# Kernel optimization log

Measured on AMD Instinct MI355X. Metric: run time of the kernel, lower is better.

## Reference

```python
import jax, jax.numpy as jnp
import numpy as np


def _norm(H, add):
    # Faithful port of GTN.norm: transpose, zero diagonal (optionally add self-loop),
    # row-degree inverse scaling, transpose back.
    Ht = H.T
    n = Ht.shape[0]
    eye = jnp.eye(n, dtype=H.dtype)
    Ht = Ht * (1.0 - eye) + (eye if add else 0.0)
    deg = jnp.sum(Ht, axis=1)
    dinv = jnp.where(deg == 0, 0.0, 1.0 / deg)
    return (dinv[:, None] * Ht).T


def _lstm(x, h0, c0, wih, whh, bih, bhh):
    # x: [B, S, D]; single-layer batch_first LSTM, PyTorch gate order (i, f, g, o).
    def step(carry, xt):
        h, c = carry
        gates = xt @ wih.T + h @ whh.T + bih + bhh
        i, f, g, o = jnp.split(gates, 4, axis=-1)
        i = jax.nn.sigmoid(i); f = jax.nn.sigmoid(f)
        g = jnp.tanh(g); o = jax.nn.sigmoid(o)
        c = f * c + i * g
        h = o * jnp.tanh(c)
        return (h, c), h
    (_, _), ys = jax.lax.scan(step, (h0, c0), jnp.transpose(x, (1, 0, 2)))
    return jnp.transpose(ys, (1, 0, 2))  # [B, S, U]


def _forward(A, X, seq_len, seqs, h0, c0, w1a, w1b, w2,
             gcn_w, lin1_w, lin1_b, lstm_wih, lstm_whh, lstm_bih, lstm_bhh, out_w):
    N = A.shape[0]
    B, S, _ = seqs.shape
    A4 = jnp.transpose(A, (2, 0, 1))  # [E, N, N]

    def gtconv(w):  # w: [C, E], softmax over edge-type channels
        return jnp.einsum('enm,ce->cnm', A4, jax.nn.softmax(w, axis=1))

    # layer 0 (first=True): H = conv1(A) @ conv2(A)
    H = jnp.matmul(gtconv(w1a), gtconv(w1b))  # [C, N, N]
    # layer 1: normalize per channel, then H = H_ @ conv1(A)
    Hn = jax.vmap(lambda h: _norm(h, False))(H)
    H = jnp.matmul(Hn, gtconv(w2))

    # gcn_conv per channel: relu(norm(H_c, add=True).T @ (X @ W)), concat over channels
    Hg = jax.vmap(lambda h: _norm(h, True))(H)  # [C, N, N]
    Xw = X @ gcn_w                              # [N, w_out]
    Xc = jax.nn.relu(jnp.einsum('cnm,nw->cmw', Hg, Xw))  # [C, N, w_out]
    X_ = jnp.transpose(Xc, (1, 0, 2)).reshape(N, -1) @ lin1_w.T + lin1_b  # [N, w_out]

    # ragged basket max-pool: masked segment-max over multi-hot baskets
    mask = seqs != 0                                           # [B, S, I]
    pooled = jnp.max(jnp.where(mask[:, :, :, None], X_[None, None], -jnp.inf), axis=2)
    basket_seqs = jnp.where(mask.any(axis=2)[..., None], pooled, 0.0)  # [B, S, w_out]

    lstm_out = _lstm(basket_seqs, h0[0], c0[0], lstm_wih, lstm_whh, lstm_bih, lstm_bhh)
    idx = jnp.clip(seq_len - 1, 0, S - 1)
    actual = lstm_out[jnp.arange(B), idx]      # [B, U]
    return jax.nn.sigmoid(actual @ out_w.T)    # [B, nb_items]


def setup_inputs() -> dict:
    N, E, C, WIN, WOUT, B, S, U = 2048, 4, 2, 64, 64, 16, 20, 256
    I = N  # nb_items
    key = jax.random.key(0)
    ks = jax.random.split(key, 16)
    A = jax.random.uniform(ks[0], (N, N, E), dtype=jnp.float32)
    X = jax.random.normal(ks[1], (N, WIN), dtype=jnp.float32)
    seq_len = jax.random.randint(ks[2], (B,), 1, S + 1)
    # sparse multi-hot baskets (~20 items per basket)
    seqs = (jax.random.uniform(ks[3], (B, S, I)) < 0.01).astype(jnp.int32)
    h0 = jnp.zeros((1, B, U), dtype=jnp.float32)
    c0 = jnp.zeros((1, B, U), dtype=jnp.float32)
    w1a = 0.1 * jax.random.normal(ks[4], (C, E), dtype=jnp.float32)
    w1b = 0.1 * jax.random.normal(ks[5], (C, E), dtype=jnp.float32)
    w2 = 0.1 * jax.random.normal(ks[6], (C, E), dtype=jnp.float32)
    gcn_w = jax.random.normal(ks[7], (WIN, WOUT), dtype=jnp.float32) / np.sqrt(WIN)
    lin1_w = 0.05 * jax.random.normal(ks[8], (WOUT, C * WOUT), dtype=jnp.float32)
    lin1_b = jnp.zeros((WOUT,), dtype=jnp.float32)
    lstm_wih = 0.05 * jax.random.normal(ks[9], (4 * U, WOUT), dtype=jnp.float32)
    lstm_whh = 0.05 * jax.random.normal(ks[10], (4 * U, U), dtype=jnp.float32)
    lstm_bih = jnp.zeros((4 * U,), dtype=jnp.float32)
    lstm_bhh = jnp.zeros((4 * U,), dtype=jnp.float32)
    out_w = 0.05 * jax.random.normal(ks[11], (I, U), dtype=jnp.float32)
    return {"A": A, "X": X, "seq_len": seq_len, "seqs": seqs, "h0": h0, "c0": c0,
            "w1a": w1a, "w1b": w1b, "w2": w2, "gcn_w": gcn_w,
            "lin1_w": lin1_w, "lin1_b": lin1_b, "lstm_wih": lstm_wih,
            "lstm_whh": lstm_whh, "lstm_bih": lstm_bih, "lstm_bhh": lstm_bhh,
            "out_w": out_w}


def reference(A, X, seq_len, seqs, h0, c0, w1a, w1b, w2, gcn_w, lin1_w, lin1_b,
              lstm_wih, lstm_whh, lstm_bih, lstm_bhh, out_w):
    return _forward(A, X, seq_len, seqs, h0, c0, w1a, w1b, w2, gcn_w,
                    lin1_w, lin1_b, lstm_wih, lstm_whh, lstm_bih, lstm_bhh, out_w)
```

## Files before the change

### kernel.cpp

```cpp
#include <hip/hip_runtime.h>
#include <hip/hip_fp16.h>
#include <math.h>

#define NN_ 2048
#define EE_ 4
#define CC_ 2
#define BB_ 16
#define SS_ 20
#define UU_ 256

#define LREGB 80
#define LLDSB 48

typedef __attribute__((ext_vector_type(8))) short short8;
typedef __attribute__((ext_vector_type(4))) float f32x4;
typedef _Float16 half2v __attribute__((ext_vector_type(2)));

__device__ __forceinline__ float sigmoidf_(float x){ return 1.f/(1.f+expf(-x)); }

__device__ __forceinline__ unsigned short f2bf(float x){
    union { float f; unsigned int u; } v; v.f = x;
    unsigned int u = v.u;
    unsigned int r = u + 0x7FFFu + ((u >> 16) & 1u);
    return (unsigned short)(r >> 16);
}

__device__ __forceinline__ half2v u2h2(unsigned int u){
    union { unsigned int u; half2v h; } c; c.u = u; return c.h;
}

__device__ __forceinline__ float dot2f(unsigned int w, unsigned int h, float acc){
#if __has_builtin(__builtin_amdgcn_fdot2)
    return __builtin_amdgcn_fdot2(u2h2(w), u2h2(h), acc, false);
#else
    float w0 = __half2float(__ushort_as_half((unsigned short)(w & 0xffffu)));
    float w1 = __half2float(__ushort_as_half((unsigned short)(w >> 16)));
    float h0f = __half2float(__ushort_as_half((unsigned short)(h & 0xffffu)));
    float h1f = __half2float(__ushort_as_half((unsigned short)(h >> 16)));
    return fmaf(w1, h1f, fmaf(w0, h0f, acc));
#endif
}

__device__ __forceinline__ float sigf(float x){
    x = fminf(fmaxf(x, -30.f), 30.f);
    float e = __builtin_amdgcn_exp2f(-1.442695041f * x);
    return __builtin_amdgcn_rcpf(1.f + e);
}
__device__ __forceinline__ float tanhf_(float x){
    x = fminf(fmaxf(x, -15.f), 15.f);
    float e = __builtin_amdgcn_exp2f(2.885390082f * x);
    return (e - 1.f) * __builtin_amdgcn_rcpf(e + 1.f);
}

typedef const __attribute__((address_space(1))) unsigned int* gas_ptr;
typedef __attribute__((address_space(3))) unsigned int* las_ptr;
__device__ __forceinline__ void gl_lds16(const void* g, void* l){
    __builtin_amdgcn_global_load_lds((gas_ptr)g, (las_ptr)l, 16, 0, 0);
}

__global__ void k_softmax(const float* __restrict__ w1a, const float* __restrict__ w1b,
                          const float* __restrict__ w2, float* __restrict__ sm){
    int t = threadIdx.x;
    if (t < 6){
        int widx = t >> 1, c = t & 1;
        const float* w = (widx==0)? w1a : ((widx==1)? w1b : w2);
        float v[EE_]; float m = -1e30f;
        for (int e=0;e<EE_;e++){ v[e]=w[c*EE_+e]; m=fmaxf(m,v[e]); }
        float s=0.f;
        for (int e=0;e<EE_;e++){ v[e]=expf(v[e]-m); s+=v[e]; }
        for (int e=0;e<EE_;e++) sm[widx*8 + c*4 + e] = v[e]/s;
    }
}

__global__ __launch_bounds__(256) void k_conv_bf16(const float4* __restrict__ A4,
        const float* __restrict__ sm, unsigned short* __restrict__ convA,
        unsigned short* __restrict__ convBT, unsigned short* __restrict__ convCT){
    __shared__ float4 tile[32][33];
    int bx = blockIdx.x*32, by = blockIdx.y*32;
    int tx = threadIdx.x & 31, ty = threadIdx.x >> 5;
    #pragma unroll
    for (int i=0;i<32;i+=8){
        int n = by+ty+i, m = bx+tx;
        float4 a = A4[(size_t)n*NN_ + m];
        tile[ty+i][tx] = a;
        #pragma unroll
        for (int cc=0;cc<CC_;cc++){
            const float* s = sm + cc*4;
            convA[(size_t)cc*NN_*NN_ + (size_t)n*NN_ + m] =
                f2bf(a.x*s[0]+a.y*s[1]+a.z*s[2]+a.w*s[3]);
        }
    }
    __syncthreads();
    #pragma unroll
    for (int i=0;i<32;i+=8){
        int x = bx+ty+i, y = by+tx;
        float4 a = tile[tx][ty+i];
        #pragma unroll
        for (int cc=0;cc<CC_;cc++){
            const float* s1 = sm + 8 + cc*4;
            const float* s2 = sm + 16 + cc*4;
            convBT[(size_t)cc*NN_*NN_ + (size_t)x*NN_ + y] =
                f2bf(a.x*s1[0]+a.y*s1[1]+a.z*s1[2]+a.w*s1[3]);
            convCT[(size_t)cc*NN_*NN_ + (size_t)x*NN_ + y] =
                f2bf(a.x*s2[0]+a.y*s2[1]+a.z*s2[2]+a.w*s2[3]);
        }
    }
}

__global__ __launch_bounds__(256) void k_mfma_gemm(const unsigned short* __restrict__ Abase,
        const unsigned short* __restrict__ Bbase, float* __restrict__ Cbase){
    const int c = blockIdx.z;
    const unsigned short* Ag = Abase + (size_t)c*NN_*NN_;
    const unsigned short* Bg = Bbase + (size_t)c*NN_*NN_;
    float* Cg = Cbase + (size_t)c*NN_*NN_;

    __shared__ __align__(16) unsigned short As[128*32];
    __shared__ __align__(16) unsigned short Bs[128*32];

    const int t = threadIdx.x;
    const int wave = t >> 6, lane = t & 63;
    const int m0 = blockIdx.y*128, n0 = blockIdx.x*128;
    const int wm = wave >> 1, wn = wave & 1;

    f32x4 acc[4][4];
    const f32x4 z = {0.f,0.f,0.f,0.f};
    #pragma unroll
    for (int i=0;i<4;i++)
        #pragma unroll
        for (int j=0;j<4;j++) acc[i][j] = z;

    const int srow = wave*32 + (lane>>2);
    const int scol = (lane&3)*8;
    const unsigned short* agp0 = Ag + (size_t)(m0+srow)*NN_ + scol;
    const unsigned short* agp1 = agp0 + (size_t)16*NN_;
    const unsigned short* bgp0 = Bg + (size_t)(n0+srow)*NN_ + scol;
    const unsigned short* bgp1 = bgp0 + (size_t)16*NN_;
    unsigned short* alp0 = &As[wave*1024];
    unsigned short* alp1 = &As[wave*1024 + 512];
    unsigned short* blp0 = &Bs[wave*1024];
    unsigned short* blp1 = &Bs[wave*1024 + 512];

    const int fr = lane & 15;
    const int fk = (lane >> 4) * 8;

    for (int k0=0; k0<NN_; k0+=32){
        gl_lds16(agp0, alp0);
        gl_lds16(agp1, alp1);
        gl_lds16(bgp0, blp0);
        gl_lds16(bgp1, blp1);
        agp0 += 32; agp1 += 32; bgp0 += 32; bgp1 += 32;
        __syncthreads();
        short8 af[4], bf[4];
        #pragma unroll
        for (int i=0;i<4;i++){
            af[i] = *(const short8*)&As[(wm*64 + i*16 + fr)*32 + fk];
            bf[i] = *(const short8*)&Bs[(wn*64 + i*16 + fr)*32 + fk];
        }
        #pragma unroll
        for (int i=0;i<4;i++)
            #pragma unroll
            for (int j=0;j<4;j++)
                acc[i][j] = __builtin_amdgcn_mfma_f32_16x16x32_bf16(af[i], bf[j], acc[i][j], 0, 0, 0);
        __syncthreads();
    }

    #pragma unroll
    for (int i=0;i<4;i++){
        int row = m0 + wm*64 + i*16 + (lane>>4)*4;
        #pragma unroll
        for (int j=0;j<4;j++){
            int col = n0 + wn*64 + j*16 + (lane & 15);
            #pragma unroll
            for (int r=0;r<4;r++)
                Cg[(size_t)(row+r)*NN_ + col] = acc[i][j][r];
        }
    }
}

__global__ __launch_bounds__(256) void k_hn(const float* __restrict__ H1,
        const float* __restrict__ dinv, unsigned short* __restrict__ Hn){
    int id = blockIdx.x*256 + threadIdx.x;
    int c = id >> 20;
    int rem = id & ((NN_*NN_/4)-1);
    int m = rem >> 9;
    int k4 = (rem & (NN_/4 - 1)) * 4;
    float4 h = *(const float4*)&H1[(size_t)c*NN_*NN_ + (size_t)m*NN_ + k4];
    float4 d = *(const float4*)&dinv[c*NN_ + k4];
    ushort4 o;
    o.x = f2bf((m==k4  ) ? 0.f : h.x*d.x);
    o.y = f2bf((m==k4+1) ? 0.f : h.y*d.y);
    o.z = f2bf((m==k4+2) ? 0.f : h.z*d.z);
    o.w = f2bf((m==k4+3) ? 0.f : h.w*d.w);
    *(ushort4*)&Hn[(size_t)c*NN_*NN_ + (size_t)m*NN_ + k4] = o;
}

__global__ __launch_bounds__(256) void k_colsum(const float* __restrict__ H, float* __restrict__ acc){
    int c = blockIdx.z;
    int m = blockIdx.x*256 + threadIdx.x;
    int nbeg = blockIdx.y*128;
    const float* Hc = H + (size_t)c*NN_*NN_;
    float s = 0.f;
    for (int n=nbeg;n<nbeg+128;n++) s += Hc[(size_t)n*NN_ + m];
    atomicAdd(&acc[c*NN_+m], s);
}

template<bool ADD>
__global__ void k_dinv(float* acc, const float* __restrict__ H){
    int id = blockIdx.x*256 + threadIdx.x;
    int c = id / NN_, m = id % NN_;
    float diag = H[(size_t)c*NN_*NN_ + (size_t)m*NN_ + m];
    float s = acc[id] - diag + (ADD ? 1.f : 0.f);
    acc[id] = (s==0.f) ? 0.f : 1.f/s;
}

__global__ __launch_bounds__(256) void k_xw(const float* __restrict__ X, const float* __restrict__ W,
                                            float* __restrict__ Xw){
    __shared__ float Ws[64*64];
    int t = threadIdx.x;
    for (int i=t;i<4096;i+=256) Ws[i]=W[i];
    __syncthreads();
    int id = blockIdx.x*256 + t;
    int n = id >> 6, w = id & 63;
    float s = 0.f;
    #pragma unroll 8
    for (int j=0;j<64;j++) s = fmaf(X[n*64+j], Ws[j*64+w], s);
    Xw[id] = s;
}

__global__ __launch_bounds__(256) void k_gcn(const float* __restrict__ H2, const float* __restrict__ Xw,
                                             float* __restrict__ Y){
    int c = blockIdx.z;
    int m0 = blockIdx.y*64;
    int n0 = blockIdx.x*256;
    const float* Hc = H2 + (size_t)c*NN_*NN_;
    __shared__ float Hs[16][68];
    __shared__ float Xs[16][68];
    int t = threadIdx.x;
    int tm = t>>4, tn = t&15;
    float acc[4][4] = {};
    for (int nb=n0; nb<n0+256; nb+=16){
        int row = t>>4, c4 = (t&15)<<2;
        *(float4*)&Hs[row][c4] = *(const float4*)&Hc[(size_t)(nb+row)*NN_ + m0 + c4];
        *(float4*)&Xs[row][c4] = *(const float4*)&Xw[(nb+row)*64 + c4];
        __syncthreads();
        #pragma unroll
        for (int k=0;k<16;k++){
            float4 av = *(const float4*)&Hs[k][tm*4];
            float4 bv = *(const float4*)&Xs[k][tn*4];
            float a[4] = {av.x,av.y,av.z,av.w};
            float b[4] = {bv.x,bv.y,bv.z,bv.w};
            #pragma unroll
            for (int i=0;i<4;i++)
                #pragma unroll
                for (int j=0;j<4;j++)
                    acc[i][j] = fmaf(a[i], b[j], acc[i][j]);
        }
        __syncthreads();
    }
    #pragma unroll
    for (int i=0;i<4;i++)
        #pragma unroll
        for (int j=0;j<4;j++)
            atomicAdd(&Y[((size_t)c*NN_ + m0+tm*4+i)*64 + tn*4+j], acc[i][j]);
}

__global__ void k_gcn_epi(const float* __restrict__ Y, const float* __restrict__ H2,
                          const float* __restrict__ Xw, const float* __restrict__ dinv2,
                          float* __restrict__ Xcat){
    int id = blockIdx.x*256 + threadIdx.x;
    int c = id >> 17;
    int rem = id & 131071;
    int m = rem >> 6, w = rem & 63;
    float diag = H2[(size_t)c*NN_*NN_ + (size_t)m*NN_ + m];
    float xwv = Xw[m*64+w];
    float v = dinv2[c*NN_+m] * (Y[id] - diag*xwv + xwv);
    Xcat[m*128 + c*64 + w] = fmaxf(v, 0.f);
}

__global__ __launch_bounds__(256) void k_lin1(const float* __restrict__ Xcat, const float* __restrict__ W,
                                              const float* __restrict__ b, float* __restrict__ Xf){
    __shared__ float WT[128*64];
    __shared__ float bs[64];
    int t = threadIdx.x;
    for (int i=t;i<8192;i+=256){ int o = i>>7, j = i&127; WT[j*64+o] = W[i]; }
    if (t<64) bs[t]=b[t];
    __syncthreads();
    int id = blockIdx.x*256 + t;
    int m = id>>6, o = id&63;
    float s = bs[o];
    #pragma unroll 8
    for (int j=0;j<128;j++) s = fmaf(Xcat[m*128+j], WT[j*64+o], s);
    Xf[id] = s;
}

__global__ __launch_bounds__(256) void k_pool(const int* __restrict__ seqs, const float* __restrict__ Xf,
                                              float* __restrict__ bask){
    int bs_id = blockIdx.x;
    __shared__ int idxbuf[NN_];
    __shared__ int cnt;
    __shared__ float red[4][64];
    int t = threadIdx.x;
    if (t==0) cnt=0;
    __syncthreads();
    const int* row = seqs + (size_t)bs_id*NN_;
    for (int i=t;i<NN_;i+=256){
        if (row[i] != 0){ int p = atomicAdd(&cnt,1); idxbuf[p]=i; }
    }
    __syncthreads();
    int nc = cnt;
    int g = t>>6, w = t&63;
    float mx = -INFINITY;
    for (int p=g;p<nc;p+=4) mx = fmaxf(mx, Xf[idxbuf[p]*64 + w]);
    red[g][w]=mx;
    __syncthreads();
    if (t<64){
        float m = fmaxf(fmaxf(red[0][t],red[1][t]),fmaxf(red[2][t],red[3][t]));
        bask[bs_id*64+t] = (nc>0)? m : 0.f;
    }
}

__global__ void k_transpose(const float* __restrict__ src, float* __restrict__ dst, int R, int Cc){
    __shared__ float tile[32][33];
    int bx = blockIdx.x*32, by = blockIdx.y*32;
    int tx = threadIdx.x, ty = threadIdx.y;
    #pragma unroll
    for (int i=0;i<32;i+=8) tile[ty+i][tx] = src[(size_t)(by+ty+i)*Cc + bx+tx];
    __syncthreads();
    #pragma unroll
    for (int i=0;i<32;i+=8) dst[(size_t)(bx+ty+i)*R + by+tx] = tile[tx][ty+i];
}

__global__ __launch_bounds__(256) void k_packw2(const float* __restrict__ whh, unsigned int* __restrict__ W2k){
    int id = blockIdx.x*256 + threadIdx.x;
    int rem = id >> 7;
    int jp  = id & 127;
    float2 v = *(const float2*)&whh[(size_t)rem*256 + 2*jp];
    unsigned int lo = __half_as_ushort(__float2half(v.x));
    unsigned int hi = __half_as_ushort(__float2half(v.y));
    W2k[id] = lo | (hi << 16);
}

__global__ __launch_bounds__(256) void k_gih(const float* __restrict__ bask, const float* __restrict__ wihT,
                                             const float* __restrict__ bih, const float* __restrict__ bhh,
                                             float* __restrict__ G){
    int id = blockIdx.x*256 + threadIdx.x;
    int r = id >> 10, o = id & 1023;
    float s = bih[o] + bhh[o];
    #pragma unroll 8
    for (int j=0;j<64;j++) s = fmaf(bask[r*64+j], wihT[j*1024+o], s);
    G[id] = s;
}

__global__ __launch_bounds__(512) void k_lstm3(const unsigned int* __restrict__ W2k,
        const float* __restrict__ G, const float* __restrict__ h0, const float* __restrict__ c0,
        const int* __restrict__ seqlen, float* __restrict__ actual){
    const int b = blockIdx.x;
    const int t = threadIdx.x;
    const int u = t & 255;
    const int half_ = t >> 8;
    const int g0 = 2*half_;
    const int g1 = g0 + 1;

    __shared__ unsigned int Wl[LLDSB][2][256];
    __shared__ unsigned int hpk[128];
    __shared__ float xg[256], xo[256];

    for (int k=0;k<LLDSB;k++){
        int idx = k*512 + t;
        int jj = idx >> 9, rem = idx & 511;
        int hf = rem >> 8, uu = rem & 255;
        ((unsigned int*)Wl)[idx] = W2k[(size_t)((2*hf+1)*256 + uu)*128 + LREGB + jj];
    }
    unsigned int wA[128], wB[LREGB];
    const unsigned int* pA = W2k + (size_t)(g0*256 + u)*128;
    const unsigned int* pB = W2k + (size_t)(g1*256 + u)*128;
    #pragma unroll
    for (int jp=0;jp<128;jp++) wA[jp] = pA[jp];
    #pragma unroll
    for (int jp=0;jp<LREGB;jp++) wB[jp] = pB[jp];

    float cv = 0.f;
    if (half_==0){
        cv = c0[b*256+u];
        ((__half*)hpk)[u] = __float2half(h0[b*256+u]);
    }
    int sl = seqlen[b]-1;
    int idx_b = sl<0?0:(sl>SS_-1?SS_-1:sl);
    __syncthreads();

    const float* gbase = G + (size_t)b*SS_*1024;
    for (int s=0;s<SS_;s++){
        float gA = gbase[s*1024 + g0*256 + u];
        float gB = gbase[s*1024 + g1*256 + u];
        float aA[4] = {0.f,0.f,0.f,0.f};
        float aB[4] = {0.f,0.f,0.f,0.f};
        #pragma unroll
        for (int jp=0;jp<128;jp++){
            unsigned int hp = hpk[jp];
            aA[jp&3] = dot2f(wA[jp], hp, aA[jp&3]);
            unsigned int wb = (jp < LREGB) ? wB[jp] : Wl[jp-LREGB][half_][u];
            aB[jp&3] = dot2f(wb, hp, aB[jp&3]);
        }
        float accA = (aA[0]+aA[1]) + (aA[2]+aA[3]) + gA;
        float accB = (aB[0]+aB[1]) + (aB[2]+aB[3]) + gB;
        float iv = 0.f, fv = 0.f;
        if (half_){
            xg[u] = tanhf_(accA);
            xo[u] = sigf(accB);
        } else {
            iv = sigf(accA);
            fv = sigf(accB);
        }
        __syncthreads();
        if (!half_){
            cv = fv*cv + iv*xg[u];
            float hv = xo[u]*tanhf_(cv);
            if (s==idx_b) actual[b*256+u] = hv;
            ((__half*)hpk)[u] = __float2half(hv);
        }
        __syncthreads();
    }
}

__global__ __launch_bounds__(256) void k_final(const float* __restrict__ actual, const float* __restrict__ owT,
                                               float* __restrict__ out){
    __shared__ float as_[256];
    int t = threadIdx.x;
    int b = blockIdx.x >> 3;
    int i0 = (blockIdx.x & 7) * 256;
    as_[t] = actual[b*256+t];
    __syncthreads();
    int i = i0 + t;
    float s = 0.f;
    #pragma unroll 8
    for (int u=0;u<256;u++) s = fmaf(as_[u], owT[u*2048 + i], s);
    out[b*2048 + i] = 1.f/(1.f+expf(-s));
}

extern "C" void kernel_launch(void* const* d_in, const int* in_sizes, int n_in,
                              void* d_out, int out_size, void* d_ws, size_t ws_size,
                              hipStream_t stream){
    const float* A     = (const float*)d_in[0];
    const float* X     = (const float*)d_in[1];
    const int*   seqln = (const int*)  d_in[2];
    const int*   seqs  = (const int*)  d_in[3];
    const float* h0    = (const float*)d_in[4];
    const float* c0    = (const float*)d_in[5];
    const float* w1a   = (const float*)d_in[6];
    const float* w1b   = (const float*)d_in[7];
    const float* w2    = (const float*)d_in[8];
    const float* gcn_w = (const float*)d_in[9];
    const float* lin1w = (const float*)d_in[10];
    const float* lin1b = (const float*)d_in[11];
    const float* wih   = (const float*)d_in[12];
    const float* whh   = (const float*)d_in[13];
    const float* bih   = (const float*)d_in[14];
    const float* bhh   = (const float*)d_in[15];
    const float* out_w = (const float*)d_in[16];
    float* out = (float*)d_out;

    char* ws = (char*)d_ws;
    size_t off = 0;
    auto alloc = [&](size_t bytes)->char*{
        char* p = ws + off; off += (bytes + 255) & ~(size_t)255; return p;
    };
    float* sm     = (float*)alloc(24*4);
    float* dinv1  = (float*)alloc(CC_*NN_*4);
    float* dinv2  = (float*)alloc(CC_*NN_*4);
    float* Xw     = (float*)alloc((size_t)NN_*64*4);
    float* Xcat   = (float*)alloc((size_t)NN_*128*4);
    float* Xf     = (float*)alloc((size_t)NN_*64*4);
    float* Ybuf   = (float*)alloc((size_t)CC_*NN_*64*4);
    float* bask   = (float*)alloc((size_t)BB_*SS_*64*4);
    float* Gih    = (float*)alloc((size_t)BB_*SS_*1024*4);
    unsigned int* W2k = (unsigned int*)alloc((size_t)1024*128*4);
    float* wihT   = (float*)alloc((size_t)64*1024*4);
    float* owT    = (float*)alloc((size_t)256*2048*4);
    float* actual = (float*)alloc((size_t)BB_*UU_*4);
    unsigned short* convA  = (unsigned short*)alloc((size_t)CC_*NN_*NN_*2);
    unsigned short* convBT = (unsigned short*)alloc((size_t)CC_*NN_*NN_*2);
    unsigned short* convCT = (unsigned short*)alloc((size_t)CC_*NN_*NN_*2);
    unsigned short* HnB    = (unsigned short*)alloc((size_t)CC_*NN_*NN_*2);
    float*          H1     = (float*)alloc((size_t)CC_*NN_*NN_*4);
    float*          H2     = (float*)convA;

    hipMemsetAsync(dinv1, 0, CC_*NN_*4, stream);
    hipMemsetAsync(dinv2, 0, CC_*NN_*4, stream);
    hipMemsetAsync(Ybuf,  0, (size_t)CC_*NN_*64*4, stream);

    k_softmax<<<1,64,0,stream>>>(w1a,w1b,w2,sm);
    k_conv_bf16<<<dim3(64,64),256,0,stream>>>((const float4*)A, sm, convA, convBT, convCT);
    k_mfma_gemm<<<dim3(16,16,2),256,0,stream>>>(convA, convBT, H1);
    k_colsum<<<dim3(8,16,2),256,0,stream>>>(H1, dinv1);
    k_dinv<false><<<CC_*NN_/256,256,0,stream>>>(dinv1, H1);
    k_hn<<<CC_*NN_*NN_/4/256,256,0,stream>>>(H1, dinv1, HnB);
    k_mfma_gemm<<<dim3(16,16,2),256,0,stream>>>(HnB, convCT, H2);
    k_colsum<<<dim3(8,16,2),256,0,stream>>>(H2, dinv2);
    k_dinv<true><<<CC_*NN_/256,256,0,stream>>>(dinv2, H2);
    k_xw<<<NN_*64/256,256,0,stream>>>(X, gcn_w, Xw);
    k_gcn<<<dim3(8,32,2),256,0,stream>>>(H2, Xw, Ybuf);
    k_gcn_epi<<<CC_*NN_*64/256,256,0,stream>>>(Ybuf, H2, Xw, dinv2, Xcat);
    k_lin1<<<NN_*64/256,256,0,stream>>>(Xcat, lin1w, lin1b, Xf);
    k_pool<<<BB_*SS_,256,0,stream>>>(seqs, Xf, bask);
    k_packw2<<<1024*128/256,256,0,stream>>>(whh, W2k);
    k_transpose<<<dim3(64/32, 1024/32),dim3(32,8),0,stream>>>(wih,  wihT, 1024, 64);
    k_transpose<<<dim3(256/32,2048/32),dim3(32,8),0,stream>>>(out_w, owT, 2048, 256);
    k_gih<<<BB_*SS_*1024/256,256,0,stream>>>(bask, wihT, bih, bhh, Gih);
    k_lstm3<<<BB_,512,0,stream>>>(W2k, Gih, h0, c0, seqln, actual);
    k_final<<<BB_*2048/256,256,0,stream>>>(actual, owT, out);
}
```

Baseline: 439.0 us.

## Fuse column sums into GEMM epilogue and store intermediates as bf16

The MFMA GEMM epilogue now writes its output as bf16 and accumulates per-column sums with atomics, so the separate column-sum kernels go away. Downstream kernels (dinv, hn, gcn, gcn_epi) read bf16 H instead of fp32, halving that memory traffic. The LSTM loop is also split so the register part and the LDS part no longer share a per-iteration select, and it gets a launch-bounds occupancy hint. Storing H as bf16 loses precision in the degree normalisation and GCN inputs, and the many column atomics could contend.

```diff
diff --git a/kernel.cpp b/kernel.cpp
--- a/kernel.cpp
+++ b/kernel.cpp
@@ -16,13 +16,14 @@
 typedef __attribute__((ext_vector_type(4))) float f32x4;
 typedef _Float16 half2v __attribute__((ext_vector_type(2)));
 
-__device__ __forceinline__ float sigmoidf_(float x){ return 1.f/(1.f+expf(-x)); }
-
 __device__ __forceinline__ unsigned short f2bf(float x){
     union { float f; unsigned int u; } v; v.f = x;
     unsigned int u = v.u;
     unsigned int r = u + 0x7FFFu + ((u >> 16) & 1u);
     return (unsigned short)(r >> 16);
+}
+__device__ __forceinline__ float bf2f(unsigned short s){
+    union { unsigned int u; float f; } v; v.u = ((unsigned int)s) << 16; return v.f;
 }
 
 __device__ __forceinline__ half2v u2h2(unsigned int u){
@@ -108,11 +109,13 @@
 }
 
 __global__ __launch_bounds__(256) void k_mfma_gemm(const unsigned short* __restrict__ Abase,
-        const unsigned short* __restrict__ Bbase, float* __restrict__ Cbase){
+        const unsigned short* __restrict__ Bbase, unsigned short* __restrict__ Cbase,
+        float* __restrict__ colbase){
     const int c = blockIdx.z;
     const unsigned short* Ag = Abase + (size_t)c*NN_*NN_;
     const unsigned short* Bg = Bbase + (size_t)c*NN_*NN_;
-    float* Cg = Cbase + (size_t)c*NN_*NN_;
+    unsigned short* Cg = Cbase + (size_t)c*NN_*NN_;
+    float* colacc = colbase + c*NN_;
 
     __shared__ __align__(16) unsigned short As[128*32];
     __shared__ __align__(16) unsigned short Bs[128*32];
@@ -165,52 +168,46 @@
     }
 
     #pragma unroll
-    for (int i=0;i<4;i++){
-        int row = m0 + wm*64 + i*16 + (lane>>4)*4;
-        #pragma unroll
-        for (int j=0;j<4;j++){
-            int col = n0 + wn*64 + j*16 + (lane & 15);
+    for (int j=0;j<4;j++){
+        int col = n0 + wn*64 + j*16 + (lane & 15);
+        float cs = 0.f;
+        #pragma unroll
+        for (int i=0;i<4;i++){
+            int row = m0 + wm*64 + i*16 + (lane>>4)*4;
             #pragma unroll
-            for (int r=0;r<4;r++)
-                Cg[(size_t)(row+r)*NN_ + col] = acc[i][j][r];
-        }
-    }
-}
-
-__global__ __launch_bounds__(256) void k_hn(const float* __restrict__ H1,
+            for (int r=0;r<4;r++){
+                Cg[(size_t)(row+r)*NN_ + col] = f2bf(acc[i][j][r]);
+                cs += acc[i][j][r];
+            }
+        }
+        atomicAdd(&colacc[col], cs);
+    }
+}
+
+template<bool ADD>
+__global__ void k_dinv(float* acc, const unsigned short* __restrict__ H){
+    int id = blockIdx.x*256 + threadIdx.x;
+    int c = id / NN_, m = id % NN_;
+    float diag = bf2f(H[(size_t)c*NN_*NN_ + (size_t)m*NN_ + m]);
+    float s = acc[id] - diag + (ADD ? 1.f : 0.f);
+    acc[id] = (s==0.f) ? 0.f : 1.f/s;
+}
+
+__global__ __launch_bounds__(256) void k_hn(const unsigned short* __restrict__ H1,
         const float* __restrict__ dinv, unsigned short* __restrict__ Hn){
     int id = blockIdx.x*256 + threadIdx.x;
     int c = id >> 20;
     int rem = id & ((NN_*NN_/4)-1);
     int m = rem >> 9;
     int k4 = (rem & (NN_/4 - 1)) * 4;
-    float4 h = *(const float4*)&H1[(size_t)c*NN_*NN_ + (size_t)m*NN_ + k4];
+    ushort4 h = *(const ushort4*)&H1[(size_t)c*NN_*NN_ + (size_t)m*NN_ + k4];
     float4 d = *(const float4*)&dinv[c*NN_ + k4];
     ushort4 o;
-    o.x = f2bf((m==k4  ) ? 0.f : h.x*d.x);
-    o.y = f2bf((m==k4+1) ? 0.f : h.y*d.y);
-    o.z = f2bf((m==k4+2) ? 0.f : h.z*d.z);
-    o.w = f2bf((m==k4+3) ? 0.f : h.w*d.w);
+    o.x = f2bf((m==k4  ) ? 0.f : bf2f(h.x)*d.x);
+    o.y = f2bf((m==k4+1) ? 0.f : bf2f(h.y)*d.y);
+    o.z = f2bf((m==k4+2) ? 0.f : bf2f(h.z)*d.z);
+    o.w = f2bf((m==k4+3) ? 0.f : bf2f(h.w)*d.w);
     *(ushort4*)&Hn[(size_t)c*NN_*NN_ + (size_t)m*NN_ + k4] = o;
-}
-
-__global__ __launch_bounds__(256) void k_colsum(const float* __restrict__ H, float* __restrict__ acc){
-    int c = blockIdx.z;
-    int m = blockIdx.x*256 + threadIdx.x;
-    int nbeg = blockIdx.y*128;
-    const float* Hc = H + (size_t)c*NN_*NN_;
-    float s = 0.f;
-    for (int n=nbeg;n<nbeg+128;n++) s += Hc[(size_t)n*NN_ + m];
-    atomicAdd(&acc[c*NN_+m], s);
-}
-
-template<bool ADD>
-__global__ void k_dinv(float* acc, const float* __restrict__ H){
-    int id = blockIdx.x*256 + threadIdx.x;
-    int c = id / NN_, m = id % NN_;
-    float diag = H[(size_t)c*NN_*NN_ + (size_t)m*NN_ + m];
-    float s = acc[id] - diag + (ADD ? 1.f : 0.f);
-    acc[id] = (s==0.f) ? 0.f : 1.f/s;
 }
 
 __global__ __launch_bounds__(256) void k_xw(const float* __restrict__ X, const float* __restrict__ W,
@@ -227,12 +224,12 @@
     Xw[id] = s;
 }
 
-__global__ __launch_bounds__(256) void k_gcn(const float* __restrict__ H2, const float* __restrict__ Xw,
-                                             float* __restrict__ Y){
+__global__ __launch_bounds__(256) void k_gcn(const unsigned short* __restrict__ H2,
+                                             const float* __restrict__ Xw, float* __restrict__ Y){
     int c = blockIdx.z;
     int m0 = blockIdx.y*64;
     int n0 = blockIdx.x*256;
-    const float* Hc = H2 + (size_t)c*NN_*NN_;
+    const unsigned short* Hc = H2 + (size_t)c*NN_*NN_;
     __shared__ float Hs[16][68];
     __shared__ float Xs[16][68];
     int t = threadIdx.x;
@@ -240,7 +237,9 @@
     float acc[4][4] = {};
     for (int nb=n0; nb<n0+256; nb+=16){
         int row = t>>4, c4 = (t&15)<<2;
-        *(float4*)&Hs[row][c4] = *(const float4*)&Hc[(size_t)(nb+row)*NN_ + m0 + c4];
+        ushort4 h4 = *(const ushort4*)&Hc[(size_t)(nb+row)*NN_ + m0 + c4];
+        Hs[row][c4+0]=bf2f(h4.x); Hs[row][c4+1]=bf2f(h4.y);
+        Hs[row][c4+2]=bf2f(h4.z); Hs[row][c4+3]=bf2f(h4.w);
         *(float4*)&Xs[row][c4] = *(const float4*)&Xw[(nb+row)*64 + c4];
         __syncthreads();
         #pragma unroll
@@ -264,14 +263,14 @@
             atomicAdd(&Y[((size_t)c*NN_ + m0+tm*4+i)*64 + tn*4+j], acc[i][j]);
 }
 
-__global__ void k_gcn_epi(const float* __restrict__ Y, const float* __restrict__ H2,
+__global__ void k_gcn_epi(const float* __restrict__ Y, const unsigned short* __restrict__ H2,
                           const float* __restrict__ Xw, const float* __restrict__ dinv2,
                           float* __restrict__ Xcat){
     int id = blockIdx.x*256 + threadIdx.x;
     int c = id >> 17;
     int rem = id & 131071;
     int m = rem >> 6, w = rem & 63;
-    float diag = H2[(size_t)c*NN_*NN_ + (size_t)m*NN_ + m];
+    float diag = bf2f(H2[(size_t)c*NN_*NN_ + (size_t)m*NN_ + m]);
     float xwv = Xw[m*64+w];
     float v = dinv2[c*NN_+m] * (Y[id] - diag*xwv + xwv);
     Xcat[m*128 + c*64 + w] = fmaxf(v, 0.f);
@@ -351,7 +350,7 @@
     G[id] = s;
 }
 
-__global__ __launch_bounds__(512) void k_lstm3(const unsigned int* __restrict__ W2k,
+__global__ __launch_bounds__(512, 2) void k_lstm4(const unsigned int* __restrict__ W2k,
         const float* __restrict__ G, const float* __restrict__ h0, const float* __restrict__ c0,
         const int* __restrict__ seqlen, float* __restrict__ actual){
     const int b = blockIdx.x;
@@ -395,11 +394,16 @@
         float aA[4] = {0.f,0.f,0.f,0.f};
         float aB[4] = {0.f,0.f,0.f,0.f};
         #pragma unroll
-        for (int jp=0;jp<128;jp++){
+        for (int jp=0;jp<LREGB;jp++){
             unsigned int hp = hpk[jp];
             aA[jp&3] = dot2f(wA[jp], hp, aA[jp&3]);
-            unsigned int wb = (jp < LREGB) ? wB[jp] : Wl[jp-LREGB][half_][u];
-            aB[jp&3] = dot2f(wb, hp, aB[jp&3]);
+            aB[jp&3] = dot2f(wB[jp], hp, aB[jp&3]);
+        }
+        #pragma unroll
+        for (int jp=LREGB;jp<128;jp++){
+            unsigned int hp = hpk[jp];
+            aA[jp&3] = dot2f(wA[jp], hp, aA[jp&3]);
+            aB[jp&3] = dot2f(Wl[jp-LREGB][half_][u], hp, aB[jp&3]);
         }
         float accA = (aA[0]+aA[1]) + (aA[2]+aA[3]) + gA;
         float accB = (aB[0]+aB[1]) + (aB[2]+aB[3]) + gB;
@@ -481,8 +485,8 @@
     unsigned short* convBT = (unsigned short*)alloc((size_t)CC_*NN_*NN_*2);
     unsigned short* convCT = (unsigned short*)alloc((size_t)CC_*NN_*NN_*2);
     unsigned short* HnB    = (unsigned short*)alloc((size_t)CC_*NN_*NN_*2);
-    float*          H1     = (float*)alloc((size_t)CC_*NN_*NN_*4);
-    float*          H2     = (float*)convA;
+    unsigned short* H1b    = (unsigned short*)alloc((size_t)CC_*NN_*NN_*2);
+    unsigned short* H2b    = convA;
 
     hipMemsetAsync(dinv1, 0, CC_*NN_*4, stream);
     hipMemsetAsync(dinv2, 0, CC_*NN_*4, stream);
@@ -490,22 +494,20 @@
 
     k_softmax<<<1,64,0,stream>>>(w1a,w1b,w2,sm);
     k_conv_bf16<<<dim3(64,64),256,0,stream>>>((const float4*)A, sm, convA, convBT, convCT);
-    k_mfma_gemm<<<dim3(16,16,2),256,0,stream>>>(convA, convBT, H1);
-    k_colsum<<<dim3(8,16,2),256,0,stream>>>(H1, dinv1);
-    k_dinv<false><<<CC_*NN_/256,256,0,stream>>>(dinv1, H1);
-    k_hn<<<CC_*NN_*NN_/4/256,256,0,stream>>>(H1, dinv1, HnB);
-    k_mfma_gemm<<<dim3(16,16,2),256,0,stream>>>(HnB, convCT, H2);
-    k_colsum<<<dim3(8,16,2),256,0,stream>>>(H2, dinv2);
-    k_dinv<true><<<CC_*NN_/256,256,0,stream>>>(dinv2, H2);
+    k_mfma_gemm<<<dim3(16,16,2),256,0,stream>>>(convA, convBT, H1b, dinv1);
+    k_dinv<false><<<CC_*NN_/256,256,0,stream>>>(dinv1, H1b);
+    k_hn<<<CC_*NN_*NN_/4/256,256,0,stream>>>(H1b, dinv1, HnB);
+    k_mfma_gemm<<<dim3(16,16,2),256,0,stream>>>(HnB, convCT, H2b, dinv2);
+    k_dinv<true><<<CC_*NN_/256,256,0,stream>>>(dinv2, H2b);
     k_xw<<<NN_*64/256,256,0,stream>>>(X, gcn_w, Xw);
-    k_gcn<<<dim3(8,32,2),256,0,stream>>>(H2, Xw, Ybuf);
-    k_gcn_epi<<<CC_*NN_*64/256,256,0,stream>>>(Ybuf, H2, Xw, dinv2, Xcat);
+    k_gcn<<<dim3(8,32,2),256,0,stream>>>(H2b, Xw, Ybuf);
+    k_gcn_epi<<<CC_*NN_*64/256,256,0,stream>>>(Ybuf, H2b, Xw, dinv2, Xcat);
     k_lin1<<<NN_*64/256,256,0,stream>>>(Xcat, lin1w, lin1b, Xf);
     k_pool<<<BB_*SS_,256,0,stream>>>(seqs, Xf, bask);
     k_packw2<<<1024*128/256,256,0,stream>>>(whh, W2k);
     k_transpose<<<dim3(64/32, 1024/32),dim3(32,8),0,stream>>>(wih,  wihT, 1024, 64);
     k_transpose<<<dim3(256/32,2048/32),dim3(32,8),0,stream>>>(out_w, owT, 2048, 256);
     k_gih<<<BB_*SS_*1024/256,256,0,stream>>>(bask, wihT, bih, bhh, Gih);
-    k_lstm3<<<BB_,512,0,stream>>>(W2k, Gih, h0, c0, seqln, actual);
+    k_lstm4<<<BB_,512,0,stream>>>(W2k, Gih, h0, c0, seqln, actual);
     k_final<<<BB_*2048/256,256,0,stream>>>(actual, owT, out);
 }
```

Result: slower. 463.6 us (+5.6%).
